# Kernel tuning notes

Hardware: AMD Instinct MI355X
Metric: run time of the kernel (lower is better)

The kernel has to match this reference:

```python
import jax, jax.numpy as jnp
import numpy as np

NUM_BOND_TYPE = 6
NUM_BOND_DIRECTION = 3
N_NODES = 20000
N_EDGES = 320000
HIDDEN = 256
OUT = 256
N_MASK = 2000


def setup_inputs() -> dict:
    key = jax.random.key(0)
    ks = jax.random.split(key, 12)
    x = jax.random.normal(ks[0], (N_NODES, HIDDEN), dtype=jnp.float32)
    edge_index = jax.random.randint(ks[1], (2, N_EDGES), 0, N_NODES, dtype=jnp.int64)
    edge_attr = jax.random.randint(ks[2], (N_EDGES, 2), 0, 3, dtype=jnp.int64)
    mask_node_indices = jax.random.randint(ks[3], (N_MASK,), 0, N_NODES, dtype=jnp.int64)
    # parameters (torch Linear convention: y = x @ W.T + b)
    def xavier(k, shape):
        fan_in, fan_out = shape[1], shape[0]
        lim = float(np.sqrt(6.0 / (fan_in + fan_out)))
        return jax.random.uniform(k, shape, jnp.float32, -lim, lim)
    prelu_a = jnp.asarray(0.25, dtype=jnp.float32)  # torch PReLU default
    W_enc = xavier(ks[4], (HIDDEN, HIDDEN))          # enc_to_dec, no bias
    E1 = xavier(ks[5], (NUM_BOND_TYPE, HIDDEN))
    E2 = xavier(ks[6], (NUM_BOND_DIRECTION, HIDDEN))
    W1 = xavier(ks[7], (2 * HIDDEN, HIDDEN))
    b1 = jnp.zeros((2 * HIDDEN,), jnp.float32)
    W2 = xavier(ks[8], (OUT, 2 * HIDDEN))
    b2 = jnp.zeros((OUT,), jnp.float32)
    return {"x": x, "edge_index": edge_index, "edge_attr": edge_attr,
            "mask_node_indices": mask_node_indices, "prelu_a": prelu_a,
            "W_enc": W_enc, "E1": E1, "E2": E2,
            "W1": W1, "b1": b1, "W2": W2, "b2": b2}


def reference(x, edge_index, edge_attr, mask_node_indices, prelu_a,
              W_enc, E1, E2, W1, b1, W2, b2):
    N = x.shape[0]
    # PReLU -> enc_to_dec linear (no bias) -> zero masked rows
    x = jnp.where(x >= 0, x, prelu_a * x)
    x = x @ W_enc.T
    x = x.at[mask_node_indices].set(0.0)
    # add self loops: (i,i) edges with attr (4, 0)
    loop = jnp.arange(N, dtype=edge_index.dtype)
    ei = jnp.concatenate([edge_index, jnp.stack([loop, loop])], axis=1)  # [2, E+N]
    loop_attr = jnp.concatenate(
        [jnp.full((N, 1), 4, edge_attr.dtype), jnp.zeros((N, 1), edge_attr.dtype)], axis=1)
    ea = jnp.concatenate([edge_attr, loop_attr], axis=0)                 # [E+N, 2]
    edge_emb = E1[ea[:, 0]] + E2[ea[:, 1]]                               # [E+N, D]
    src, dst = ei[0], ei[1]                                              # j -> i
    msg = x[src] + edge_emb                                              # [E+N, D]
    aggr = jax.ops.segment_sum(msg, dst, num_segments=N)                 # [N, D]
    # GIN MLP: Linear -> ReLU -> Linear
    h = jax.nn.relu(aggr @ W1.T + b1)
    return h @ W2.T + b2
```

## Files before the change

### kernel.cpp

```cpp
#include <hip/hip_runtime.h>

#define HIDDEN 256
#define CAP 64

typedef _Float16 h4_t __attribute__((ext_vector_type(4)));
typedef _Float16 h8_t __attribute__((ext_vector_type(8)));
typedef float    f4_t __attribute__((ext_vector_type(4)));

typedef const __attribute__((address_space(1))) void* gbl_ptr_t;
typedef __attribute__((address_space(3))) void*       lds_ptr_t;

__device__ inline f4_t cvt4(h4_t h) {
    f4_t o; o.x = (float)h.x; o.y = (float)h.y; o.z = (float)h.z; o.w = (float)h.w;
    return o;
}

__global__ __launch_bounds__(256) void k_prep(
        const float* __restrict__ x, _Float16* __restrict__ xh,
        const float* __restrict__ prelu_a, int M, int Mpad, int nb_x,
        const int* __restrict__ ei, const int* __restrict__ ea, int E,
        int* __restrict__ cnt, int* __restrict__ csr, int nb_fill,
        const float* __restrict__ W_enc, const float* __restrict__ W1,
        const float* __restrict__ W2, _Float16* __restrict__ Whenc,
        _Float16* __restrict__ Wh1, _Float16* __restrict__ Wh2, int nb_w,
        const int* __restrict__ mask, unsigned char* __restrict__ flags, int NM) {
    int b = blockIdx.x;
    int t = threadIdx.x;
    if (b < nb_x) {
        int base = (b * 256 + t) * 4;
        if (base >= Mpad * HIDDEN) return;
        int row = base >> 8;
        h4_t o;
        if (row < M) {
            float pa = *prelu_a;
            f4_t v = *(const f4_t*)(x + base);
            o.x = (_Float16)(v.x >= 0.f ? v.x : pa * v.x);
            o.y = (_Float16)(v.y >= 0.f ? v.y : pa * v.y);
            o.z = (_Float16)(v.z >= 0.f ? v.z : pa * v.z);
            o.w = (_Float16)(v.w >= 0.f ? v.w : pa * v.w);
        } else {
            o = (h4_t)(_Float16)0.f;
        }
        *(h4_t*)(xh + base) = o;
        return;
    }
    b -= nb_x;
    if (b < nb_fill) {
        int e = b * 256 + t;
        if (e >= E) return;
        int src = ei[e];
        int dst = ei[E + e];
        int combo = ea[2 * e] * 3 + ea[2 * e + 1];
        int slot = atomicAdd(&cnt[dst], 1);
        if (slot < CAP) csr[dst * CAP + slot] = src | (combo << 16);
        return;
    }
    b -= nb_fill;
    if (b < nb_w) {
        const int n0 = HIDDEN * HIDDEN, n1 = 2 * HIDDEN * HIDDEN, n2 = HIDDEN * 2 * HIDDEN;
        int base = (b * 256 + t) * 4;
        const float* s; _Float16* d; int off;
        if (base < n0) { s = W_enc; d = Whenc; off = base; }
        else if (base < n0 + n1) { s = W1; d = Wh1; off = base - n0; }
        else if (base < n0 + n1 + n2) { s = W2; d = Wh2; off = base - n0 - n1; }
        else return;
        f4_t v = *(const f4_t*)(s + off);
        h4_t o; o.x = (_Float16)v.x; o.y = (_Float16)v.y;
        o.z = (_Float16)v.z; o.w = (_Float16)v.w;
        *(h4_t*)(d + off) = o;
        return;
    }
    b -= nb_w;
    {
        int i = b * 256 + t;
        if (i < NM) flags[mask[i]] = 1;
    }
}

__global__ __launch_bounds__(256) void k_aggregate(
        const _Float16* __restrict__ xe,
        const float* __restrict__ E1, const float* __restrict__ E2,
        const int* __restrict__ cnt, const int* __restrict__ csr,
        _Float16* __restrict__ aggr, int N, int Mpad) {
    __shared__ __align__(16) _Float16 e12h[18 * HIDDEN];
    int t = threadIdx.x;
    for (int idx = t; idx < 18 * 64; idx += 256) {
        int combo = idx >> 6, c4 = (idx & 63) * 4;
        int a1 = combo / 3, a2 = combo - a1 * 3;
        f4_t v1 = *(const f4_t*)(E1 + a1 * HIDDEN + c4);
        f4_t v2 = *(const f4_t*)(E2 + a2 * HIDDEN + c4);
        h4_t o;
        o.x = (_Float16)(v1.x + v2.x); o.y = (_Float16)(v1.y + v2.y);
        o.z = (_Float16)(v1.z + v2.z); o.w = (_Float16)(v1.w + v2.w);
        *(h4_t*)(e12h + combo * HIDDEN + c4) = o;
    }
    __syncthreads();
    int node = blockIdx.x * 4 + (t >> 6);
    if (node >= Mpad) return;
    int lane = t & 63;
    int c0 = lane * 4;
    if (node >= N) {
        *(h4_t*)(aggr + (size_t)node * HIDDEN + c0) = (h4_t)(_Float16)0.f;
        return;
    }
    int deg = cnt[node];
    if (deg > CAP) deg = CAP;
    const int* lst = csr + (size_t)node * CAP;
    int pv = (lane < deg) ? lst[lane] : 0;

    h4_t hs = *(const h4_t*)(xe + (size_t)node * HIDDEN + c0);
    h4_t se = *(const h4_t*)(e12h + 12 * HIDDEN + c0);
    f4_t acc = cvt4(hs) + cvt4(se);

    int e = 0;
    for (; e + 7 < deg; e += 8) {
        int p[8]; h4_t hv[8], qv[8];
#pragma unroll
        for (int j = 0; j < 8; ++j) p[j] = __shfl(pv, e + j, 64);
#pragma unroll
        for (int j = 0; j < 8; ++j)
            hv[j] = *(const h4_t*)(xe + (size_t)(p[j] & 0xFFFF) * HIDDEN + c0);
#pragma unroll
        for (int j = 0; j < 8; ++j)
            qv[j] = *(const h4_t*)(e12h + (p[j] >> 16) * HIDDEN + c0);
        h4_t s0 = (hv[0] + qv[0]) + (hv[1] + qv[1]);
        h4_t s1 = (hv[2] + qv[2]) + (hv[3] + qv[3]);
        h4_t s2 = (hv[4] + qv[4]) + (hv[5] + qv[5]);
        h4_t s3 = (hv[6] + qv[6]) + (hv[7] + qv[7]);
        acc += cvt4(s0) + cvt4(s1);
        acc += cvt4(s2) + cvt4(s3);
    }
    for (; e < deg; ++e) {
        int p = __shfl(pv, e, 64);
        h4_t h = *(const h4_t*)(xe + (size_t)(p & 0xFFFF) * HIDDEN + c0);
        h4_t q = *(const h4_t*)(e12h + (p >> 16) * HIDDEN + c0);
        acc += cvt4(h + q);
    }
    h4_t o;
    o.x = (_Float16)acc.x; o.y = (_Float16)acc.y;
    o.z = (_Float16)acc.z; o.w = (_Float16)acc.w;
    *(h4_t*)(aggr + (size_t)node * HIDDEN + c0) = o;
}

template <int TM, int K, bool RELU, bool HAS_BIAS, bool OUT_F16, bool MASK>
__global__ __launch_bounds__(64) void k_gemm64(
        const _Float16* __restrict__ A, const _Float16* __restrict__ B,
        const float* __restrict__ bias, void* __restrict__ Cout,
        const unsigned char* __restrict__ flags, int Mstore, int N) {
    constexpr int BM = TM * 16;
    constexpr int LPS = TM + 4;
    __shared__ __align__(16) _Float16 As[2][BM * 32];
    __shared__ __align__(16) _Float16 Bs[2][64 * 32];
    int L = threadIdx.x;
    int m0 = blockIdx.x * BM, n0 = blockIdx.y * 64;
    int lr = L & 15, lk = (L >> 4) * 8;

    f4_t acc[TM][4] = {};

    auto stage = [&](int k0, int buf) {
#pragma unroll
        for (int i = 0; i < TM; ++i) {
            int c = L + 64 * i;
            __builtin_amdgcn_global_load_lds(
                (gbl_ptr_t)(A + (size_t)(m0 + (c >> 2)) * K + k0 + (c & 3) * 8),
                (lds_ptr_t)(&As[buf][c * 8]), 16, 0, 0);
        }
#pragma unroll
        for (int i = 0; i < 4; ++i) {
            int c = L + 64 * i;
            __builtin_amdgcn_global_load_lds(
                (gbl_ptr_t)(B + (size_t)(n0 + (c >> 2)) * K + k0 + (c & 3) * 8),
                (lds_ptr_t)(&Bs[buf][c * 8]), 16, 0, 0);
        }
    };

    constexpr int NS = K / 32;
    stage(0, 0);
    if (NS > 1) stage(32, 1);
#pragma unroll
    for (int s = 0; s < NS; ++s) {
        int buf = s & 1;
        if (s + 1 < NS) {
            asm volatile("s_waitcnt vmcnt(%0)" :: "i"(LPS) : "memory");
        } else {
            asm volatile("s_waitcnt vmcnt(0)" ::: "memory");
        }
        h8_t af[TM], bf[4];
#pragma unroll
        for (int i = 0; i < TM; ++i) af[i] = *(const h8_t*)&As[buf][(i * 16 + lr) * 32 + lk];
#pragma unroll
        for (int j = 0; j < 4; ++j)  bf[j] = *(const h8_t*)&Bs[buf][(j * 16 + lr) * 32 + lk];
        asm volatile("s_waitcnt lgkmcnt(0)" ::: "memory");
        if (s + 2 < NS) stage((s + 2) * 32, buf);
#pragma unroll
        for (int i = 0; i < TM; ++i)
#pragma unroll
            for (int j = 0; j < 4; ++j)
                acc[i][j] = __builtin_amdgcn_mfma_f32_16x16x32_f16(af[i], bf[j], acc[i][j], 0, 0, 0);
    }

    int lr4 = (L >> 4) * 4;
#pragma unroll
    for (int i = 0; i < TM; ++i)
#pragma unroll
        for (int r = 0; r < 4; ++r) {
            int row = m0 + i * 16 + lr4 + r;
            float zm = (MASK && flags[row]) ? 0.f : 1.f;
#pragma unroll
            for (int j = 0; j < 4; ++j) {
                int col = n0 + j * 16 + lr;
                float v = acc[i][j][r];
                if (HAS_BIAS) v += bias[col];
                if (RELU) v = v > 0.f ? v : 0.f;
                v *= zm;
                if (OUT_F16) {
                    ((_Float16*)Cout)[(size_t)row * N + col] = (_Float16)v;
                } else {
                    if (row < Mstore) ((float*)Cout)[(size_t)row * N + col] = v;
                }
            }
        }
}

extern "C" void kernel_launch(void* const* d_in, const int* in_sizes, int n_in,
                              void* d_out, int out_size, void* d_ws, size_t ws_size,
                              hipStream_t stream) {
    const float* x       = (const float*)d_in[0];
    const int*   ei      = (const int*)d_in[1];
    const int*   ea      = (const int*)d_in[2];
    const int*   mask    = (const int*)d_in[3];
    const float* prelu_a = (const float*)d_in[4];
    const float* W_enc   = (const float*)d_in[5];
    const float* E1      = (const float*)d_in[6];
    const float* E2      = (const float*)d_in[7];
    const float* W1      = (const float*)d_in[8];
    const float* b1      = (const float*)d_in[9];
    const float* W2      = (const float*)d_in[10];
    const float* b2      = (const float*)d_in[11];
    float*       out     = (float*)d_out;

    int N  = in_sizes[0] / HIDDEN;
    int E  = in_sizes[1] / 2;
    int NM = in_sizes[3];
    int Mpad = ((N + 127) / 128) * 128;

    char* ws = (char*)d_ws;
    size_t off = 0;
    _Float16* xh    = (_Float16*)(ws + off); off += (size_t)Mpad * HIDDEN * 2;
    _Float16* XEh   = (_Float16*)(ws + off); off += (size_t)Mpad * HIDDEN * 2;
    _Float16* AGh   = (_Float16*)(ws + off); off += (size_t)Mpad * HIDDEN * 2;
    _Float16* Hh    = (_Float16*)(ws + off); off += (size_t)Mpad * 2 * HIDDEN * 2;
    _Float16* Whenc = (_Float16*)(ws + off); off += (size_t)HIDDEN * HIDDEN * 2;
    _Float16* Wh1   = (_Float16*)(ws + off); off += (size_t)2 * HIDDEN * HIDDEN * 2;
    _Float16* Wh2   = (_Float16*)(ws + off); off += (size_t)HIDDEN * 2 * HIDDEN * 2;
    int* cnt        = (int*)(ws + off);      off += (size_t)N * 4;
    unsigned char* flags = (unsigned char*)(ws + off); off += (size_t)Mpad;
    off = (off + 15) & ~(size_t)15;
    int* csr        = (int*)(ws + off);      off += (size_t)N * CAP * 4;

    hipMemsetAsync(cnt, 0, (size_t)N * 4 + (size_t)Mpad, stream);

    int nb_x    = (Mpad * HIDDEN / 4 + 255) / 256;
    int nb_fill = (E + 255) / 256;
    int wtot4   = (HIDDEN * HIDDEN + 2 * HIDDEN * HIDDEN + HIDDEN * 2 * HIDDEN) / 4;
    int nb_w    = (wtot4 + 255) / 256;
    int nb_m    = (NM + 255) / 256;
    k_prep<<<nb_x + nb_fill + nb_w + nb_m, 256, 0, stream>>>(
        x, xh, prelu_a, N, Mpad, nb_x,
        ei, ea, E, cnt, csr, nb_fill,
        W_enc, W1, W2, Whenc, Wh1, Wh2, nb_w,
        mask, flags, NM);

    dim3 g1(Mpad / 32, HIDDEN / 64);
    k_gemm64<2, HIDDEN, false, false, true, true><<<g1, 64, 0, stream>>>(
        xh, Whenc, nullptr, XEh, flags, N, HIDDEN);

    k_aggregate<<<(Mpad + 3) / 4, 256, 0, stream>>>(XEh, E1, E2, cnt, csr, AGh, N, Mpad);

    dim3 g2(Mpad / 32, 2 * HIDDEN / 64);
    k_gemm64<2, HIDDEN, true, true, true, false><<<g2, 64, 0, stream>>>(
        AGh, Wh1, b1, Hh, nullptr, N, 2 * HIDDEN);

    dim3 g3(Mpad / 32, HIDDEN / 64);
    k_gemm64<2, 2 * HIDDEN, false, true, false, false><<<g3, 64, 0, stream>>>(
        Hh, Wh2, b2, out, nullptr, N, HIDDEN);
}
```

Measured before the change: 186.1 us.

## Fold encoder weight into first MLP layer and drop encoder GEMM

The message sum is split into two parts, which relies on linearity. One part sums the masked, PReLU'd node features. The other sums the edge embeddings. The two are written side by side into a 512-wide buffer. A small in-kernel matmul in the prep kernel builds the concatenated weight [W1·W_enc | W1], so a single GEMM with K=512 replaces the separate enc_to_dec GEMM plus the W1 GEMM. Masking moves from the GEMM epilogue into the aggregation as flag lookups. This removes one kernel launch and the full write and read of the intermediate projected features. In exchange, the first MLP GEMM does more work, the aggregation output is twice as wide, and the folded weights are rounded to fp16.

```diff
diff --git a/kernel.cpp b/kernel.cpp
--- a/kernel.cpp
+++ b/kernel.cpp
@@ -20,10 +20,11 @@
         const float* __restrict__ prelu_a, int M, int Mpad, int nb_x,
         const int* __restrict__ ei, const int* __restrict__ ea, int E,
         int* __restrict__ cnt, int* __restrict__ csr, int nb_fill,
-        const float* __restrict__ W_enc, const float* __restrict__ W1,
-        const float* __restrict__ W2, _Float16* __restrict__ Whenc,
-        _Float16* __restrict__ Wh1, _Float16* __restrict__ Wh2, int nb_w,
+        const float* __restrict__ W1, const float* __restrict__ W2,
+        _Float16* __restrict__ Bcat, _Float16* __restrict__ Wh2, int nb_w,
+        const float* __restrict__ W_enc, int nb_wc,
         const int* __restrict__ mask, unsigned char* __restrict__ flags, int NM) {
+    __shared__ float W1s[8 * HIDDEN];
     int b = blockIdx.x;
     int t = threadIdx.x;
     if (b < nb_x) {
@@ -57,20 +58,42 @@
     }
     b -= nb_fill;
     if (b < nb_w) {
-        const int n0 = HIDDEN * HIDDEN, n1 = 2 * HIDDEN * HIDDEN, n2 = HIDDEN * 2 * HIDDEN;
+        const int n1 = 2 * HIDDEN * HIDDEN;
+        const int n2 = HIDDEN * 2 * HIDDEN;
         int base = (b * 256 + t) * 4;
-        const float* s; _Float16* d; int off;
-        if (base < n0) { s = W_enc; d = Whenc; off = base; }
-        else if (base < n0 + n1) { s = W1; d = Wh1; off = base - n0; }
-        else if (base < n0 + n1 + n2) { s = W2; d = Wh2; off = base - n0 - n1; }
-        else return;
-        f4_t v = *(const f4_t*)(s + off);
-        h4_t o; o.x = (_Float16)v.x; o.y = (_Float16)v.y;
-        o.z = (_Float16)v.z; o.w = (_Float16)v.w;
-        *(h4_t*)(d + off) = o;
+        if (base < n1) {
+            int row = base >> 8, col = base & 255;
+            f4_t v = *(const f4_t*)(W1 + base);
+            h4_t o; o.x = (_Float16)v.x; o.y = (_Float16)v.y;
+            o.z = (_Float16)v.z; o.w = (_Float16)v.w;
+            *(h4_t*)(Bcat + (size_t)row * 512 + 256 + col) = o;
+        } else if (base < n1 + n2) {
+            int off = base - n1;
+            f4_t v = *(const f4_t*)(W2 + off);
+            h4_t o; o.x = (_Float16)v.x; o.y = (_Float16)v.y;
+            o.z = (_Float16)v.z; o.w = (_Float16)v.w;
+            *(h4_t*)(Wh2 + off) = o;
+        }
         return;
     }
     b -= nb_w;
+    if (b < nb_wc) {
+        int n0 = b * 8;
+        for (int i = t; i < 8 * HIDDEN; i += 256) W1s[i] = W1[n0 * HIDDEN + i];
+        __syncthreads();
+        int k = t;
+        float acc[8] = {};
+        for (int c = 0; c < HIDDEN; ++c) {
+            float we = W_enc[c * HIDDEN + k];
+#pragma unroll
+            for (int r = 0; r < 8; ++r) acc[r] += W1s[r * HIDDEN + c] * we;
+        }
+#pragma unroll
+        for (int r = 0; r < 8; ++r)
+            Bcat[(size_t)(n0 + r) * 512 + k] = (_Float16)acc[r];
+        return;
+    }
+    b -= nb_wc;
     {
         int i = b * 256 + t;
         if (i < NM) flags[mask[i]] = 1;
@@ -78,10 +101,11 @@
 }
 
 __global__ __launch_bounds__(256) void k_aggregate(
-        const _Float16* __restrict__ xe,
+        const _Float16* __restrict__ xp,
         const float* __restrict__ E1, const float* __restrict__ E2,
         const int* __restrict__ cnt, const int* __restrict__ csr,
-        _Float16* __restrict__ aggr, int N, int Mpad) {
+        const unsigned char* __restrict__ flags,
+        _Float16* __restrict__ Acat, int N, int Mpad) {
     __shared__ __align__(16) _Float16 e12h[18 * HIDDEN];
     int t = threadIdx.x;
     for (int idx = t; idx < 18 * 64; idx += 256) {
@@ -99,18 +123,25 @@
     if (node >= Mpad) return;
     int lane = t & 63;
     int c0 = lane * 4;
+    const h4_t hz = (h4_t)(_Float16)0.f;
     if (node >= N) {
-        *(h4_t*)(aggr + (size_t)node * HIDDEN + c0) = (h4_t)(_Float16)0.f;
+        *(h4_t*)(Acat + (size_t)node * 512 + c0) = hz;
+        *(h4_t*)(Acat + (size_t)node * 512 + 256 + c0) = hz;
         return;
     }
     int deg = cnt[node];
     if (deg > CAP) deg = CAP;
     const int* lst = csr + (size_t)node * CAP;
-    int pv = (lane < deg) ? lst[lane] : 0;
-
-    h4_t hs = *(const h4_t*)(xe + (size_t)node * HIDDEN + c0);
-    h4_t se = *(const h4_t*)(e12h + 12 * HIDDEN + c0);
-    f4_t acc = cvt4(hs) + cvt4(se);
+    int pv = 0;
+    if (lane < deg) {
+        pv = lst[lane];
+        pv |= ((int)flags[pv & 0xFFFF]) << 21;
+    }
+
+    h4_t hs = *(const h4_t*)(xp + (size_t)node * HIDDEN + c0);
+    if (flags[node]) hs = hz;
+    f4_t accS = cvt4(hs);
+    f4_t accE = cvt4(*(const h4_t*)(e12h + 12 * HIDDEN + c0));
 
     int e = 0;
     for (; e + 7 < deg; e += 8) {
@@ -118,35 +149,42 @@
 #pragma unroll
         for (int j = 0; j < 8; ++j) p[j] = __shfl(pv, e + j, 64);
 #pragma unroll
+        for (int j = 0; j < 8; ++j) {
+            h4_t h = *(const h4_t*)(xp + (size_t)(p[j] & 0xFFFF) * HIDDEN + c0);
+            hv[j] = (p[j] >> 21) ? hz : h;
+        }
+#pragma unroll
         for (int j = 0; j < 8; ++j)
-            hv[j] = *(const h4_t*)(xe + (size_t)(p[j] & 0xFFFF) * HIDDEN + c0);
-#pragma unroll
-        for (int j = 0; j < 8; ++j)
-            qv[j] = *(const h4_t*)(e12h + (p[j] >> 16) * HIDDEN + c0);
-        h4_t s0 = (hv[0] + qv[0]) + (hv[1] + qv[1]);
-        h4_t s1 = (hv[2] + qv[2]) + (hv[3] + qv[3]);
-        h4_t s2 = (hv[4] + qv[4]) + (hv[5] + qv[5]);
-        h4_t s3 = (hv[6] + qv[6]) + (hv[7] + qv[7]);
-        acc += cvt4(s0) + cvt4(s1);
-        acc += cvt4(s2) + cvt4(s3);
+            qv[j] = *(const h4_t*)(e12h + ((p[j] >> 16) & 0x1F) * HIDDEN + c0);
+        h4_t s0 = (hv[0] + hv[1]) + (hv[2] + hv[3]);
+        h4_t s1 = (hv[4] + hv[5]) + (hv[6] + hv[7]);
+        h4_t q0 = (qv[0] + qv[1]) + (qv[2] + qv[3]);
+        h4_t q1 = (qv[4] + qv[5]) + (qv[6] + qv[7]);
+        accS += cvt4(s0) + cvt4(s1);
+        accE += cvt4(q0) + cvt4(q1);
     }
     for (; e < deg; ++e) {
         int p = __shfl(pv, e, 64);
-        h4_t h = *(const h4_t*)(xe + (size_t)(p & 0xFFFF) * HIDDEN + c0);
-        h4_t q = *(const h4_t*)(e12h + (p >> 16) * HIDDEN + c0);
-        acc += cvt4(h + q);
-    }
-    h4_t o;
-    o.x = (_Float16)acc.x; o.y = (_Float16)acc.y;
-    o.z = (_Float16)acc.z; o.w = (_Float16)acc.w;
-    *(h4_t*)(aggr + (size_t)node * HIDDEN + c0) = o;
-}
-
-template <int TM, int K, bool RELU, bool HAS_BIAS, bool OUT_F16, bool MASK>
+        h4_t h = *(const h4_t*)(xp + (size_t)(p & 0xFFFF) * HIDDEN + c0);
+        if (p >> 21) h = hz;
+        h4_t q = *(const h4_t*)(e12h + ((p >> 16) & 0x1F) * HIDDEN + c0);
+        accS += cvt4(h);
+        accE += cvt4(q);
+    }
+    h4_t oS, oE;
+    oS.x = (_Float16)accS.x; oS.y = (_Float16)accS.y;
+    oS.z = (_Float16)accS.z; oS.w = (_Float16)accS.w;
+    oE.x = (_Float16)accE.x; oE.y = (_Float16)accE.y;
+    oE.z = (_Float16)accE.z; oE.w = (_Float16)accE.w;
+    *(h4_t*)(Acat + (size_t)node * 512 + c0) = oS;
+    *(h4_t*)(Acat + (size_t)node * 512 + 256 + c0) = oE;
+}
+
+template <int TM, int K, bool RELU, bool HAS_BIAS, bool OUT_F16>
 __global__ __launch_bounds__(64) void k_gemm64(
         const _Float16* __restrict__ A, const _Float16* __restrict__ B,
         const float* __restrict__ bias, void* __restrict__ Cout,
-        const unsigned char* __restrict__ flags, int Mstore, int N) {
+        int Mstore, int N) {
     constexpr int BM = TM * 16;
     constexpr int LPS = TM + 4;
     __shared__ __align__(16) _Float16 As[2][BM * 32];
@@ -205,14 +243,12 @@
 #pragma unroll
         for (int r = 0; r < 4; ++r) {
             int row = m0 + i * 16 + lr4 + r;
-            float zm = (MASK && flags[row]) ? 0.f : 1.f;
 #pragma unroll
             for (int j = 0; j < 4; ++j) {
                 int col = n0 + j * 16 + lr;
                 float v = acc[i][j][r];
                 if (HAS_BIAS) v += bias[col];
                 if (RELU) v = v > 0.f ? v : 0.f;
-                v *= zm;
                 if (OUT_F16) {
                     ((_Float16*)Cout)[(size_t)row * N + col] = (_Float16)v;
                 } else {
@@ -246,42 +282,39 @@
 
     char* ws = (char*)d_ws;
     size_t off = 0;
-    _Float16* xh    = (_Float16*)(ws + off); off += (size_t)Mpad * HIDDEN * 2;
-    _Float16* XEh   = (_Float16*)(ws + off); off += (size_t)Mpad * HIDDEN * 2;
-    _Float16* AGh   = (_Float16*)(ws + off); off += (size_t)Mpad * HIDDEN * 2;
-    _Float16* Hh    = (_Float16*)(ws + off); off += (size_t)Mpad * 2 * HIDDEN * 2;
-    _Float16* Whenc = (_Float16*)(ws + off); off += (size_t)HIDDEN * HIDDEN * 2;
-    _Float16* Wh1   = (_Float16*)(ws + off); off += (size_t)2 * HIDDEN * HIDDEN * 2;
-    _Float16* Wh2   = (_Float16*)(ws + off); off += (size_t)HIDDEN * 2 * HIDDEN * 2;
-    int* cnt        = (int*)(ws + off);      off += (size_t)N * 4;
+    _Float16* xh   = (_Float16*)(ws + off); off += (size_t)Mpad * HIDDEN * 2;
+    _Float16* Acat = (_Float16*)(ws + off); off += (size_t)Mpad * 512 * 2;
+    _Float16* Hh   = (_Float16*)(ws + off); off += (size_t)Mpad * 512 * 2;
+    _Float16* Bcat = (_Float16*)(ws + off); off += (size_t)512 * 512 * 2;
+    _Float16* Wh2  = (_Float16*)(ws + off); off += (size_t)HIDDEN * 512 * 2;
+    int* cnt       = (int*)(ws + off);      off += (size_t)N * 4;
     unsigned char* flags = (unsigned char*)(ws + off); off += (size_t)Mpad;
     off = (off + 15) & ~(size_t)15;
-    int* csr        = (int*)(ws + off);      off += (size_t)N * CAP * 4;
+    int* csr       = (int*)(ws + off);      off += (size_t)N * CAP * 4;
 
     hipMemsetAsync(cnt, 0, (size_t)N * 4 + (size_t)Mpad, stream);
 
     int nb_x    = (Mpad * HIDDEN / 4 + 255) / 256;
     int nb_fill = (E + 255) / 256;
-    int wtot4   = (HIDDEN * HIDDEN + 2 * HIDDEN * HIDDEN + HIDDEN * 2 * HIDDEN) / 4;
+    int wtot4   = (2 * HIDDEN * HIDDEN + HIDDEN * 2 * HIDDEN) / 4;
     int nb_w    = (wtot4 + 255) / 256;
+    int nb_wc   = 512 / 8;
     int nb_m    = (NM + 255) / 256;
-    k_prep<<<nb_x + nb_fill + nb_w + nb_m, 256, 0, stream>>>(
+    k_prep<<<nb_x + nb_fill + nb_w + nb_wc + nb_m, 256, 0, stream>>>(
         x, xh, prelu_a, N, Mpad, nb_x,
         ei, ea, E, cnt, csr, nb_fill,
-        W_enc, W1, W2, Whenc, Wh1, Wh2, nb_w,
+        W1, W2, Bcat, Wh2, nb_w,
+        W_enc, nb_wc,
         mask, flags, NM);
 
-    dim3 g1(Mpad / 32, HIDDEN / 64);
-    k_gemm64<2, HIDDEN, false, false, true, true><<<g1, 64, 0, stream>>>(
-        xh, Whenc, nullptr, XEh, flags, N, HIDDEN);
-
-    k_aggregate<<<(Mpad + 3) / 4, 256, 0, stream>>>(XEh, E1, E2, cnt, csr, AGh, N, Mpad);
-
-    dim3 g2(Mpad / 32, 2 * HIDDEN / 64);
-    k_gemm64<2, HIDDEN, true, true, true, false><<<g2, 64, 0, stream>>>(
-        AGh, Wh1, b1, Hh, nullptr, N, 2 * HIDDEN);
+    k_aggregate<<<(Mpad + 3) / 4, 256, 0, stream>>>(
+        xh, E1, E2, cnt, csr, flags, Acat, N, Mpad);
+
+    dim3 g2(Mpad / 64, 512 / 64);
+    k_gemm64<4, 512, true, true, true><<<g2, 64, 0, stream>>>(
+        Acat, Bcat, b1, Hh, N, 512);
 
     dim3 g3(Mpad / 32, HIDDEN / 64);
-    k_gemm64<2, 2 * HIDDEN, false, true, false, false><<<g3, 64, 0, stream>>>(
-        Hh, Wh2, b2, out, nullptr, N, HIDDEN);
-}
+    k_gemm64<2, 512, false, true, false><<<g3, 64, 0, stream>>>(
+        Hh, Wh2, b2, out, N, HIDDEN);
+}
```

New measurement: 207.9 us. 11.7% more time.
